# Kernel optimization log

Hardware: AMD Instinct MI355X
Metric: run time of the kernel (lower is better)

## Reference

```python
import jax, jax.numpy as jnp
import numpy as np

N = 8192
IN_F = 256
OUT_F = 128
ALPHA = 0.2  # leakyrelu slope
NEG_BIG = -9e15


def setup_inputs() -> dict:
    key = jax.random.key(0)
    k1, k2, k3, k4 = jax.random.split(key, 4)
    x = jax.random.normal(k1, (N, IN_F), dtype=jnp.float32)
    adj = (jax.random.uniform(k2, (N, N)) < 0.01).astype(jnp.float32)
    adj = jnp.maximum(adj, jnp.eye(N, dtype=jnp.float32))
    # xavier-uniform-style init scales
    W = jax.random.uniform(k3, (IN_F, OUT_F), dtype=jnp.float32,
                           minval=-1.0, maxval=1.0) * np.sqrt(6.0 / (IN_F + OUT_F))
    a = jax.random.uniform(k4, (2 * OUT_F, 1), dtype=jnp.float32,
                           minval=-1.0, maxval=1.0) * np.sqrt(6.0 / (2 * OUT_F + 1))
    return {"x": x, "adj": adj, "W": W, "a": a}


def reference(x, adj, W, a):
    # h = x @ W  -> (N, F)
    h = x @ W
    # e_ij = leakyrelu(a^T [h_i || h_j]) = leakyrelu((h @ a1)_i + (h @ a2)_j)
    # equivalent to torch's repeat/cat construction, without the N^2*2F tensor
    a1 = a[:OUT_F, 0]   # (F,)
    a2 = a[OUT_F:, 0]   # (F,)
    s1 = h @ a1         # (N,)
    s2 = h @ a2         # (N,)
    e = s1[:, None] + s2[None, :]                      # (N, N)
    e = jnp.where(e > 0, e, ALPHA * e)                 # leakyrelu
    att = jnp.where(adj > 0, e, NEG_BIG)
    att = jax.nn.softmax(att, axis=1)                  # (N, N)
    # dropout is identity in eval mode
    h_prime = att @ h                                  # (N, F)
    return jax.nn.elu(h_prime)
```

## Files before the change

kernel.cpp:

```cpp
#include <hip/hip_runtime.h>
#include <cstdint>
#include <cstddef>

#define N 8192
#define IN_F 256
#define OUT_F 128
#define ALPHA 0.2f
#define CAP 256
typedef unsigned long long ull;

__device__ __forceinline__ float bf2f(unsigned short u) {
    return __uint_as_float(((unsigned)u) << 16);
}
__device__ __forceinline__ unsigned short f2bf(float f) {
    unsigned x = __float_as_uint(f);
    unsigned r = (x + 0x7FFFu + ((x >> 16) & 1u)) >> 16;
    return (unsigned short)r;
}

__global__ __launch_bounds__(256) void gemm_xw(const float* __restrict__ x,
                                               const float* __restrict__ W,
                                               const float* __restrict__ a,
                                               unsigned short* __restrict__ hb,
                                               float* __restrict__ s1,
                                               float* __restrict__ s2) {
    __shared__ __align__(16) float xsT[64 * 36];
    __shared__ __align__(16) float ws[64 * 128];
    const int tid = threadIdx.x;
    const int R0  = blockIdx.x * 32;
    const int r0  = (tid >> 5) * 4;
    const int c0  = (tid & 31) * 4;

    float acc[4][4];
#pragma unroll
    for (int r = 0; r < 4; ++r)
#pragma unroll
        for (int c = 0; c < 4; ++c) acc[r][c] = 0.f;

    for (int k0 = 0; k0 < IN_F; k0 += 64) {
#pragma unroll
        for (int q = 0; q < 2; ++q) {
            const int f  = tid + q * 256;
            const int r  = f >> 4;
            const int k4 = f & 15;
            const float4 v = *(const float4*)(x + (size_t)(R0 + r) * IN_F + k0 + k4 * 4);
            xsT[(k4 * 4 + 0) * 36 + r] = v.x;
            xsT[(k4 * 4 + 1) * 36 + r] = v.y;
            xsT[(k4 * 4 + 2) * 36 + r] = v.z;
            xsT[(k4 * 4 + 3) * 36 + r] = v.w;
        }
#pragma unroll
        for (int q = 0; q < 8; ++q) {
            const int f = tid + q * 256;
            *(float4*)(ws + f * 4) = *(const float4*)(W + (size_t)k0 * OUT_F + f * 4);
        }
        __syncthreads();

#pragma unroll 8
        for (int kk = 0; kk < 64; ++kk) {
            const float4 wv = *(const float4*)(ws + kk * 128 + c0);
            const float4 xv = *(const float4*)(xsT + kk * 36 + r0);
            acc[0][0] += xv.x * wv.x; acc[0][1] += xv.x * wv.y; acc[0][2] += xv.x * wv.z; acc[0][3] += xv.x * wv.w;
            acc[1][0] += xv.y * wv.x; acc[1][1] += xv.y * wv.y; acc[1][2] += xv.y * wv.z; acc[1][3] += xv.y * wv.w;
            acc[2][0] += xv.z * wv.x; acc[2][1] += xv.z * wv.y; acc[2][2] += xv.z * wv.z; acc[2][3] += xv.z * wv.w;
            acc[3][0] += xv.w * wv.x; acc[3][1] += xv.w * wv.y; acc[3][2] += xv.w * wv.z; acc[3][3] += xv.w * wv.w;
        }
        __syncthreads();
    }

#pragma unroll
    for (int r = 0; r < 4; ++r) {
        ushort4 o4;
        o4.x = f2bf(acc[r][0]); o4.y = f2bf(acc[r][1]);
        o4.z = f2bf(acc[r][2]); o4.w = f2bf(acc[r][3]);
        *(ushort4*)(hb + (size_t)(R0 + r0 + r) * OUT_F + c0) = o4;
    }

    const float4 a1v = *(const float4*)(a + c0);
    const float4 a2v = *(const float4*)(a + OUT_F + c0);
#pragma unroll
    for (int r = 0; r < 4; ++r) {
        float p1 = acc[r][0] * a1v.x + acc[r][1] * a1v.y + acc[r][2] * a1v.z + acc[r][3] * a1v.w;
        float p2 = acc[r][0] * a2v.x + acc[r][1] * a2v.y + acc[r][2] * a2v.z + acc[r][3] * a2v.w;
#pragma unroll
        for (int off = 16; off > 0; off >>= 1) {
            p1 += __shfl_xor(p1, off);
            p2 += __shfl_xor(p2, off);
        }
        if ((tid & 31) == 0) {
            s1[R0 + r0 + r] = p1;
            s2[R0 + r0 + r] = p2;
        }
    }
}

__global__ __launch_bounds__(256, 8) void adj_scan(const float* __restrict__ adj,
                                                   ull* __restrict__ bm) {
    const int tid  = threadIdx.x;
    const int lane = tid & 63;
    const size_t tg = (size_t)blockIdx.x * 256 + tid;
    const float4* __restrict__ adj4 = (const float4*)adj;
#pragma unroll 8
    for (int it = 0; it < 32; ++it) {
        const size_t g = tg + (size_t)it * (2048u * 256u);
        const float4 v = adj4[g];
        const ull m0 = __ballot(v.x > 0.f);
        const ull m1 = __ballot(v.y > 0.f);
        const ull m2 = __ballot(v.z > 0.f);
        const ull m3 = __ballot(v.w > 0.f);
        if (lane < 4) {
            const ull mv = lane == 0 ? m0 : (lane == 1 ? m1 : (lane == 2 ? m2 : m3));
            bm[(g >> 6) * 4 + lane] = mv;
        }
    }
}

__global__ __launch_bounds__(256, 8) void gat_gather(const ull* __restrict__ bm,
                                                     const unsigned short* __restrict__ hb,
                                                     const float* __restrict__ s1,
                                                     const float* __restrict__ s2,
                                                     float* __restrict__ out) {
    const int tid  = threadIdx.x;
    const int wv   = tid >> 6;
    const int lane = tid & 63;
    const int row  = blockIdx.x * 4 + wv;

    __shared__ int   jl[4][CAP];
    __shared__ float el[4][CAP];

    const ull* bmrow = bm + (size_t)row * 128;
    const ulonglong2 ww = *(const ulonglong2*)(bmrow + 2 * lane);
    const int cnt = __popcll(ww.x) + __popcll(ww.y);

    int scan = cnt;
#pragma unroll
    for (int d = 1; d < 64; d <<= 1) {
        const int y = __shfl_up(scan, d);
        if (lane >= d) scan += y;
    }
    const int total = __shfl(scan, 63);
    int p = scan - cnt;
    {
        ull w = ww.x;
        const int wi = 2 * lane;
        const int base = (wi >> 2) * 256 + (wi & 3);
        while (w) {
            const int b = __builtin_ctzll(w);
            w &= w - 1;
            if (p < CAP) jl[wv][p] = base + 4 * b;
            ++p;
        }
    }
    {
        ull w = ww.y;
        const int wi = 2 * lane + 1;
        const int base = (wi >> 2) * 256 + (wi & 3);
        while (w) {
            const int b = __builtin_ctzll(w);
            w &= w - 1;
            if (p < CAP) jl[wv][p] = base + 4 * b;
            ++p;
        }
    }
    __syncthreads();
    const int n = total < CAP ? total : CAP;

    const float si = s1[row];
    float ev[4];
    float lmax = -1e30f;
#pragma unroll
    for (int t = 0; t < 4; ++t) {
        const int l = lane + t * 64;
        float e = -1e30f;
        if (l < n) {
            e = si + s2[jl[wv][l]];
            e = e > 0.f ? e : ALPHA * e;
        }
        ev[t] = e;
        lmax = fmaxf(lmax, e);
    }
#pragma unroll
    for (int off = 32; off > 0; off >>= 1) lmax = fmaxf(lmax, __shfl_xor(lmax, off));

    float dp = 0.f;
#pragma unroll
    for (int t = 0; t < 4; ++t) {
        const int l = lane + t * 64;
        if (l < n) {
            const float wgt = __expf(ev[t] - lmax);
            el[wv][l] = wgt;
            dp += wgt;
        }
    }
#pragma unroll
    for (int off = 32; off > 0; off >>= 1) dp += __shfl_xor(dp, off);
    const float denom = dp;
    __syncthreads();

    const int half = lane >> 5;
    const int col4 = (lane & 31) * 4;
    float a0 = 0.f, a1 = 0.f, a2 = 0.f, a3 = 0.f;
#pragma unroll 2
    for (int l = half; l < n; l += 2) {
        const float wgt = el[wv][l];
        const int j = jl[wv][l];
        const ushort4 hv = *(const ushort4*)(hb + (size_t)j * OUT_F + col4);
        a0 += wgt * bf2f(hv.x);
        a1 += wgt * bf2f(hv.y);
        a2 += wgt * bf2f(hv.z);
        a3 += wgt * bf2f(hv.w);
    }
    a0 += __shfl_xor(a0, 32);
    a1 += __shfl_xor(a1, 32);
    a2 += __shfl_xor(a2, 32);
    a3 += __shfl_xor(a3, 32);

    if (half == 0) {
        const float r = 1.f / denom;
        float v0 = a0 * r, v1 = a1 * r, v2 = a2 * r, v3 = a3 * r;
        float4 o;
        o.x = v0 > 0.f ? v0 : (__expf(v0) - 1.f);
        o.y = v1 > 0.f ? v1 : (__expf(v1) - 1.f);
        o.z = v2 > 0.f ? v2 : (__expf(v2) - 1.f);
        o.w = v3 > 0.f ? v3 : (__expf(v3) - 1.f);
        *(float4*)(out + (size_t)row * OUT_F + col4) = o;
    }
}

extern "C" void kernel_launch(void* const* d_in, const int* in_sizes, int n_in,
                              void* d_out, int out_size, void* d_ws, size_t ws_size,
                              hipStream_t stream) {
    const float* x   = (const float*)d_in[0];
    const float* adj = (const float*)d_in[1];
    const float* W   = (const float*)d_in[2];
    const float* a   = (const float*)d_in[3];
    float* out = (float*)d_out;

    char* wsb = (char*)d_ws;
    unsigned short* hb = (unsigned short*)wsb;
    float* s1 = (float*)(wsb + 2 * 1024 * 1024);
    float* s2 = s1 + N;
    ull*   bm = (ull*)(wsb + 2 * 1024 * 1024 + 64 * 1024);

    gemm_xw<<<N / 32, 256, 0, stream>>>(x, W, a, hb, s1, s2);
    adj_scan<<<2048, 256, 0, stream>>>(adj, bm);
    gat_gather<<<2048, 256, 0, stream>>>(bm, hb, s1, s2, out);
}
```

Before: 79.33 us.

## Merge GEMM and adjacency bitmask scan into one heterogeneous launch

Folds the x@W GEMM and the adjacency-to-bitmask scan into a single kernel. The first 256 blocks do the GEMM and the remaining 2048 blocks do the scan, so the two independent stages run concurrently instead of back to back. This also removes one launch boundary. The GEMM k-tile shrinks from 64 to 32 to cut shared memory per block and allow more co-resident scan blocks, and the adjacency reads and bitmask writes use nontemporal hints. The GEMM blocks now share a launch with the bandwidth-bound scan, which may change how the GPU schedules them.

```diff
diff --git a/kernel.cpp b/kernel.cpp
--- a/kernel.cpp
+++ b/kernel.cpp
@@ -8,6 +8,7 @@
 #define ALPHA 0.2f
 #define CAP 256
 typedef unsigned long long ull;
+typedef float f32x4 __attribute__((ext_vector_type(4)));
 
 __device__ __forceinline__ float bf2f(unsigned short u) {
     return __uint_as_float(((unsigned)u) << 16);
@@ -18,99 +19,99 @@
     return (unsigned short)r;
 }
 
-__global__ __launch_bounds__(256) void gemm_xw(const float* __restrict__ x,
-                                               const float* __restrict__ W,
-                                               const float* __restrict__ a,
-                                               unsigned short* __restrict__ hb,
-                                               float* __restrict__ s1,
-                                               float* __restrict__ s2) {
-    __shared__ __align__(16) float xsT[64 * 36];
-    __shared__ __align__(16) float ws[64 * 128];
+__global__ __launch_bounds__(256) void fused_gemm_scan(const float* __restrict__ x,
+                                                       const float* __restrict__ W,
+                                                       const float* __restrict__ a,
+                                                       const float* __restrict__ adj,
+                                                       unsigned short* __restrict__ hb,
+                                                       float* __restrict__ s1,
+                                                       float* __restrict__ s2,
+                                                       ull* __restrict__ bm) {
+    __shared__ __align__(16) float xsT[32 * 36];
+    __shared__ __align__(16) float ws2[32 * 128];
     const int tid = threadIdx.x;
-    const int R0  = blockIdx.x * 32;
-    const int r0  = (tid >> 5) * 4;
-    const int c0  = (tid & 31) * 4;
-
-    float acc[4][4];
-#pragma unroll
-    for (int r = 0; r < 4; ++r)
-#pragma unroll
-        for (int c = 0; c < 4; ++c) acc[r][c] = 0.f;
-
-    for (int k0 = 0; k0 < IN_F; k0 += 64) {
-#pragma unroll
-        for (int q = 0; q < 2; ++q) {
-            const int f  = tid + q * 256;
-            const int r  = f >> 4;
-            const int k4 = f & 15;
-            const float4 v = *(const float4*)(x + (size_t)(R0 + r) * IN_F + k0 + k4 * 4);
-            xsT[(k4 * 4 + 0) * 36 + r] = v.x;
-            xsT[(k4 * 4 + 1) * 36 + r] = v.y;
-            xsT[(k4 * 4 + 2) * 36 + r] = v.z;
-            xsT[(k4 * 4 + 3) * 36 + r] = v.w;
-        }
-#pragma unroll
-        for (int q = 0; q < 8; ++q) {
-            const int f = tid + q * 256;
-            *(float4*)(ws + f * 4) = *(const float4*)(W + (size_t)k0 * OUT_F + f * 4);
-        }
-        __syncthreads();
+
+    if (blockIdx.x < 256) {
+        const int R0 = blockIdx.x * 32;
+        const int r0 = (tid >> 5) * 4;
+        const int c0 = (tid & 31) * 4;
+
+        float acc[4][4];
+#pragma unroll
+        for (int r = 0; r < 4; ++r)
+#pragma unroll
+            for (int c = 0; c < 4; ++c) acc[r][c] = 0.f;
+
+        for (int k0 = 0; k0 < IN_F; k0 += 32) {
+            {
+                const int r  = tid >> 3;
+                const int k4 = tid & 7;
+                const float4 v = *(const float4*)(x + (size_t)(R0 + r) * IN_F + k0 + k4 * 4);
+                xsT[(k4 * 4 + 0) * 36 + r] = v.x;
+                xsT[(k4 * 4 + 1) * 36 + r] = v.y;
+                xsT[(k4 * 4 + 2) * 36 + r] = v.z;
+                xsT[(k4 * 4 + 3) * 36 + r] = v.w;
+            }
+#pragma unroll
+            for (int q = 0; q < 4; ++q) {
+                const int f = tid + q * 256;
+                *(float4*)(ws2 + f * 4) = *(const float4*)(W + (size_t)k0 * OUT_F + f * 4);
+            }
+            __syncthreads();
 
 #pragma unroll 8
-        for (int kk = 0; kk < 64; ++kk) {
-            const float4 wv = *(const float4*)(ws + kk * 128 + c0);
-            const float4 xv = *(const float4*)(xsT + kk * 36 + r0);
-            acc[0][0] += xv.x * wv.x; acc[0][1] += xv.x * wv.y; acc[0][2] += xv.x * wv.z; acc[0][3] += xv.x * wv.w;
-            acc[1][0] += xv.y * wv.x; acc[1][1] += xv.y * wv.y; acc[1][2] += xv.y * wv.z; acc[1][3] += xv.y * wv.w;
-            acc[2][0] += xv.z * wv.x; acc[2][1] += xv.z * wv.y; acc[2][2] += xv.z * wv.z; acc[2][3] += xv.z * wv.w;
-            acc[3][0] += xv.w * wv.x; acc[3][1] += xv.w * wv.y; acc[3][2] += xv.w * wv.z; acc[3][3] += xv.w * wv.w;
-        }
-        __syncthreads();
-    }
-
-#pragma unroll
-    for (int r = 0; r < 4; ++r) {
-        ushort4 o4;
-        o4.x = f2bf(acc[r][0]); o4.y = f2bf(acc[r][1]);
-        o4.z = f2bf(acc[r][2]); o4.w = f2bf(acc[r][3]);
-        *(ushort4*)(hb + (size_t)(R0 + r0 + r) * OUT_F + c0) = o4;
-    }
-
-    const float4 a1v = *(const float4*)(a + c0);
-    const float4 a2v = *(const float4*)(a + OUT_F + c0);
-#pragma unroll
-    for (int r = 0; r < 4; ++r) {
-        float p1 = acc[r][0] * a1v.x + acc[r][1] * a1v.y + acc[r][2] * a1v.z + acc[r][3] * a1v.w;
-        float p2 = acc[r][0] * a2v.x + acc[r][1] * a2v.y + acc[r][2] * a2v.z + acc[r][3] * a2v.w;
-#pragma unroll
-        for (int off = 16; off > 0; off >>= 1) {
-            p1 += __shfl_xor(p1, off);
-            p2 += __shfl_xor(p2, off);
-        }
-        if ((tid & 31) == 0) {
-            s1[R0 + r0 + r] = p1;
-            s2[R0 + r0 + r] = p2;
-        }
-    }
-}
-
-__global__ __launch_bounds__(256, 8) void adj_scan(const float* __restrict__ adj,
-                                                   ull* __restrict__ bm) {
-    const int tid  = threadIdx.x;
-    const int lane = tid & 63;
-    const size_t tg = (size_t)blockIdx.x * 256 + tid;
-    const float4* __restrict__ adj4 = (const float4*)adj;
+            for (int kk = 0; kk < 32; ++kk) {
+                const float4 wv = *(const float4*)(ws2 + kk * 128 + c0);
+                const float4 xv = *(const float4*)(xsT + kk * 36 + r0);
+                acc[0][0] += xv.x * wv.x; acc[0][1] += xv.x * wv.y; acc[0][2] += xv.x * wv.z; acc[0][3] += xv.x * wv.w;
+                acc[1][0] += xv.y * wv.x; acc[1][1] += xv.y * wv.y; acc[1][2] += xv.y * wv.z; acc[1][3] += xv.y * wv.w;
+                acc[2][0] += xv.z * wv.x; acc[2][1] += xv.z * wv.y; acc[2][2] += xv.z * wv.z; acc[2][3] += xv.z * wv.w;
+                acc[3][0] += xv.w * wv.x; acc[3][1] += xv.w * wv.y; acc[3][2] += xv.w * wv.z; acc[3][3] += xv.w * wv.w;
+            }
+            __syncthreads();
+        }
+
+#pragma unroll
+        for (int r = 0; r < 4; ++r) {
+            ushort4 o4;
+            o4.x = f2bf(acc[r][0]); o4.y = f2bf(acc[r][1]);
+            o4.z = f2bf(acc[r][2]); o4.w = f2bf(acc[r][3]);
+            *(ushort4*)(hb + (size_t)(R0 + r0 + r) * OUT_F + c0) = o4;
+        }
+
+        const float4 a1v = *(const float4*)(a + c0);
+        const float4 a2v = *(const float4*)(a + OUT_F + c0);
+#pragma unroll
+        for (int r = 0; r < 4; ++r) {
+            float p1 = acc[r][0] * a1v.x + acc[r][1] * a1v.y + acc[r][2] * a1v.z + acc[r][3] * a1v.w;
+            float p2 = acc[r][0] * a2v.x + acc[r][1] * a2v.y + acc[r][2] * a2v.z + acc[r][3] * a2v.w;
+#pragma unroll
+            for (int off = 16; off > 0; off >>= 1) {
+                p1 += __shfl_xor(p1, off);
+                p2 += __shfl_xor(p2, off);
+            }
+            if ((tid & 31) == 0) {
+                s1[R0 + r0 + r] = p1;
+                s2[R0 + r0 + r] = p2;
+            }
+        }
+    } else {
+        const int bid  = blockIdx.x - 256;
+        const int lane = tid & 63;
+        const size_t tg = (size_t)bid * 256 + tid;
+        const f32x4* __restrict__ adj4 = (const f32x4*)adj;
 #pragma unroll 8
-    for (int it = 0; it < 32; ++it) {
-        const size_t g = tg + (size_t)it * (2048u * 256u);
-        const float4 v = adj4[g];
-        const ull m0 = __ballot(v.x > 0.f);
-        const ull m1 = __ballot(v.y > 0.f);
-        const ull m2 = __ballot(v.z > 0.f);
-        const ull m3 = __ballot(v.w > 0.f);
-        if (lane < 4) {
-            const ull mv = lane == 0 ? m0 : (lane == 1 ? m1 : (lane == 2 ? m2 : m3));
-            bm[(g >> 6) * 4 + lane] = mv;
+        for (int it = 0; it < 32; ++it) {
+            const size_t g = tg + (size_t)it * (2048u * 256u);
+            const f32x4 v = __builtin_nontemporal_load(adj4 + g);
+            const ull m0 = __ballot(v.x > 0.f);
+            const ull m1 = __ballot(v.y > 0.f);
+            const ull m2 = __ballot(v.z > 0.f);
+            const ull m3 = __ballot(v.w > 0.f);
+            if (lane < 4) {
+                const ull mv = lane == 0 ? m0 : (lane == 1 ? m1 : (lane == 2 ? m2 : m3));
+                __builtin_nontemporal_store(mv, bm + (g >> 6) * 4 + lane);
+            }
         }
     }
 }
@@ -242,7 +243,6 @@
     float* s2 = s1 + N;
     ull*   bm = (ull*)(wsb + 2 * 1024 * 1024 + 64 * 1024);
 
-    gemm_xw<<<N / 32, 256, 0, stream>>>(x, W, a, hb, s1, s2);
-    adj_scan<<<2048, 256, 0, stream>>>(adj, bm);
+    fused_gemm_scan<<<256 + 2048, 256, 0, stream>>>(x, W, a, adj, hb, s1, s2, bm);
     gat_gather<<<2048, 256, 0, stream>>>(bm, hb, s1, s2, out);
 }
```

After: 90.81 us. 14.5% more time.

## Fuse adjacency scan into gather kernel with ballot-based in-wave compaction

Applied to the files above, without the earlier changes.

Removes the separate adj_scan kernel and the bitmask buffer. Each wave now reads its own adjacency row directly, with a software-prefetched double buffer, and compacts neighbor indices into shared memory using ballot and popcount. The gather loop unroll goes from 2 to 4 and the block-level __syncthreads calls are dropped, since each wave only touches its own shared rows. This saves a launch and the bitmask write and read, but the 256 MB adjacency read now happens in per-row wave-serial order instead of a flat streaming pattern.

```diff
diff --git a/kernel.cpp b/kernel.cpp
--- a/kernel.cpp
+++ b/kernel.cpp
@@ -8,6 +8,7 @@
 #define ALPHA 0.2f
 #define CAP 256
 typedef unsigned long long ull;
+typedef float f32x4 __attribute__((ext_vector_type(4)));
 
 __device__ __forceinline__ float bf2f(unsigned short u) {
     return __uint_as_float(((unsigned)u) << 16);
@@ -94,32 +95,11 @@
     }
 }
 
-__global__ __launch_bounds__(256, 8) void adj_scan(const float* __restrict__ adj,
-                                                   ull* __restrict__ bm) {
-    const int tid  = threadIdx.x;
-    const int lane = tid & 63;
-    const size_t tg = (size_t)blockIdx.x * 256 + tid;
-    const float4* __restrict__ adj4 = (const float4*)adj;
-#pragma unroll 8
-    for (int it = 0; it < 32; ++it) {
-        const size_t g = tg + (size_t)it * (2048u * 256u);
-        const float4 v = adj4[g];
-        const ull m0 = __ballot(v.x > 0.f);
-        const ull m1 = __ballot(v.y > 0.f);
-        const ull m2 = __ballot(v.z > 0.f);
-        const ull m3 = __ballot(v.w > 0.f);
-        if (lane < 4) {
-            const ull mv = lane == 0 ? m0 : (lane == 1 ? m1 : (lane == 2 ? m2 : m3));
-            bm[(g >> 6) * 4 + lane] = mv;
-        }
-    }
-}
-
-__global__ __launch_bounds__(256, 8) void gat_gather(const ull* __restrict__ bm,
-                                                     const unsigned short* __restrict__ hb,
-                                                     const float* __restrict__ s1,
-                                                     const float* __restrict__ s2,
-                                                     float* __restrict__ out) {
+__global__ __launch_bounds__(256, 8) void gat_fused(const float* __restrict__ adj,
+                                                    const unsigned short* __restrict__ hb,
+                                                    const float* __restrict__ s1,
+                                                    const float* __restrict__ s2,
+                                                    float* __restrict__ out) {
     const int tid  = threadIdx.x;
     const int wv   = tid >> 6;
     const int lane = tid & 63;
@@ -128,42 +108,41 @@
     __shared__ int   jl[4][CAP];
     __shared__ float el[4][CAP];
 
-    const ull* bmrow = bm + (size_t)row * 128;
-    const ulonglong2 ww = *(const ulonglong2*)(bmrow + 2 * lane);
-    const int cnt = __popcll(ww.x) + __popcll(ww.y);
-
-    int scan = cnt;
-#pragma unroll
-    for (int d = 1; d < 64; d <<= 1) {
-        const int y = __shfl_up(scan, d);
-        if (lane >= d) scan += y;
-    }
-    const int total = __shfl(scan, 63);
-    int p = scan - cnt;
-    {
-        ull w = ww.x;
-        const int wi = 2 * lane;
-        const int base = (wi >> 2) * 256 + (wi & 3);
-        while (w) {
-            const int b = __builtin_ctzll(w);
-            w &= w - 1;
-            if (p < CAP) jl[wv][p] = base + 4 * b;
-            ++p;
-        }
-    }
-    {
-        ull w = ww.y;
-        const int wi = 2 * lane + 1;
-        const int base = (wi >> 2) * 256 + (wi & 3);
-        while (w) {
-            const int b = __builtin_ctzll(w);
-            w &= w - 1;
-            if (p < CAP) jl[wv][p] = base + 4 * b;
-            ++p;
-        }
-    }
-    __syncthreads();
-    const int n = total < CAP ? total : CAP;
+    const f32x4* __restrict__ arow = (const f32x4*)(adj + (size_t)row * N);
+    const ull below = (1ull << lane) - 1ull;
+
+    int tot = 0;
+    f32x4 va[4], vb[4];
+#pragma unroll
+    for (int u = 0; u < 4; ++u) va[u] = arow[lane + u * 64];
+
+    for (int b = 0; b < 8; ++b) {
+        if (b < 7) {
+#pragma unroll
+            for (int u = 0; u < 4; ++u) vb[u] = arow[lane + ((b + 1) * 4 + u) * 64];
+        }
+#pragma unroll
+        for (int u = 0; u < 4; ++u) {
+            const int jb = ((b * 4 + u) * 64 + lane) * 4;
+            const float av[4] = {va[u].x, va[u].y, va[u].z, va[u].w};
+#pragma unroll
+            for (int c = 0; c < 4; ++c) {
+                const bool hit = av[c] > 0.f;
+                const ull m = __ballot(hit);
+                if (m) {
+                    const int base = tot;
+                    tot += __popcll(m);
+                    if (hit) {
+                        const int p = base + __popcll(m & below);
+                        if (p < CAP) jl[wv][p] = jb + c;
+                    }
+                }
+            }
+        }
+#pragma unroll
+        for (int u = 0; u < 4; ++u) va[u] = vb[u];
+    }
+    const int n = tot < CAP ? tot : CAP;
 
     const float si = s1[row];
     float ev[4];
@@ -195,12 +174,11 @@
 #pragma unroll
     for (int off = 32; off > 0; off >>= 1) dp += __shfl_xor(dp, off);
     const float denom = dp;
-    __syncthreads();
 
     const int half = lane >> 5;
     const int col4 = (lane & 31) * 4;
     float a0 = 0.f, a1 = 0.f, a2 = 0.f, a3 = 0.f;
-#pragma unroll 2
+#pragma unroll 4
     for (int l = half; l < n; l += 2) {
         const float wgt = el[wv][l];
         const int j = jl[wv][l];
@@ -240,9 +218,7 @@
     unsigned short* hb = (unsigned short*)wsb;
     float* s1 = (float*)(wsb + 2 * 1024 * 1024);
     float* s2 = s1 + N;
-    ull*   bm = (ull*)(wsb + 2 * 1024 * 1024 + 64 * 1024);
 
     gemm_xw<<<N / 32, 256, 0, stream>>>(x, W, a, hb, s1, s2);
-    adj_scan<<<2048, 256, 0, stream>>>(adj, bm);
-    gat_gather<<<2048, 256, 0, stream>>>(bm, hb, s1, s2, out);
-}
+    gat_fused<<<2048, 256, 0, stream>>>(adj, hb, s1, s2, out);
+}
```

Result: faster. 71.09 us (-10.4%).
